# Kernel tuning notes

Hardware: AMD Instinct MI355X
Metric: run time of the kernel (lower is better)

Reference implementation:

```python
import jax, jax.numpy as jnp
import numpy as np

N = 500_000          # total nodes (25000 graphs x 20 joints)
E = 800_000          # total edges (25000 graphs x 32 edges)
NUM_EDGES = 32       # edges per graph (module init arg)
IN_C = 128
OUT_C = 256
LN_EPS = 1e-5


def setup_inputs() -> dict:
    key = jax.random.key(0)
    ks = jax.random.split(key, 8)
    x = jax.random.normal(ks[0], (N, IN_C), dtype=jnp.float32)
    edge_index = jax.random.randint(ks[1], (2, E), 0, N, dtype=jnp.int64)
    # learned per-graph edge weights (init ones in torch; randomized positive here)
    edge_weights = jax.random.uniform(ks[2], (NUM_EDGES,), jnp.float32, 0.5, 1.5)
    W_gcn = jax.random.normal(ks[3], (IN_C, OUT_C), jnp.float32) / np.float32(np.sqrt(IN_C))
    b_gcn = jnp.zeros((OUT_C,), jnp.float32)
    W_res = jax.random.normal(ks[4], (IN_C, OUT_C), jnp.float32) / np.float32(np.sqrt(IN_C))
    b_res = jnp.zeros((OUT_C,), jnp.float32)
    gamma = jnp.ones((OUT_C,), jnp.float32)
    beta = jnp.zeros((OUT_C,), jnp.float32)
    return dict(x=x, edge_weights=edge_weights, W_gcn=W_gcn, b_gcn=b_gcn,
                W_res=W_res, b_res=b_res, gamma=gamma, beta=beta,
                edge_index=edge_index)


def reference(x, edge_weights, W_gcn, b_gcn, W_res, b_res, gamma, beta, edge_index):
    n = x.shape[0]
    e_tot = edge_index.shape[1]
    batch_size = e_tot // NUM_EDGES
    ew = jnp.tile(edge_weights, batch_size)            # repeated per-batch weights [E]
    row, col = edge_index[0], edge_index[1]            # source -> target

    # GCN symmetric normalization with implicit self loops (weight 1)
    deg = jax.ops.segment_sum(ew, col, num_segments=n) + 1.0   # [N]
    dinv = jax.lax.rsqrt(deg)                                   # [N]
    norm = dinv[row] * ew * dinv[col]                           # [E]

    xw = x @ W_gcn                                              # [N, OUT_C]
    agg = jax.ops.segment_sum(norm[:, None] * xw[row], col, num_segments=n)
    # self-loop contribution: norm_ii = dinv_i * 1 * dinv_i = 1/deg_i
    gcn_out = agg + xw * (dinv * dinv)[:, None] + b_gcn         # [N, OUT_C]

    res = x @ W_res + b_res                                     # residual Linear
    h = gcn_out + res

    mu = jnp.mean(h, axis=-1, keepdims=True)
    var = jnp.mean((h - mu) ** 2, axis=-1, keepdims=True)
    hn = (h - mu) * jax.lax.rsqrt(var + LN_EPS)
    return jax.nn.relu(hn * gamma + beta)
```

## Files before the change

### kernel.cpp

```cpp
#include <hip/hip_runtime.h>
#include <hip/hip_bf16.h>

typedef __attribute__((ext_vector_type(8))) short short8;
typedef __attribute__((ext_vector_type(8))) unsigned short ushort8;
typedef __attribute__((ext_vector_type(4))) float f32x4;
typedef unsigned short u16;

#define IN_C 128
#define OUT_C 256
#define LN_EPS 1e-5f

__device__ __forceinline__ u16 f2bf(float f) {
    __hip_bfloat16 h = __float2bfloat16(f);
    return __builtin_bit_cast(u16, h);
}

__global__ void k_count(const int* __restrict__ ei, const float* __restrict__ ew,
                        float* __restrict__ deg, int* __restrict__ cnt, int E, int nbc,
                        const float* __restrict__ Wg, const float* __restrict__ Wr,
                        const float* __restrict__ bg, const float* __restrict__ br,
                        u16* __restrict__ wfrag, float* __restrict__ bc) {
    int b = blockIdx.x;
    if (b < nbc) {
        int e = b * 256 + threadIdx.x;
        if (e < E) {
            int c = ei[E + e];
            atomicAdd(&deg[c], ew[e & 31]);
            atomicAdd(&cnt[c], 1);
        }
        return;
    }
    int tid = (b - nbc) * 256 + threadIdx.x;
    if (tid < OUT_C) bc[tid] = bg[tid] + br[tid];
    if (tid >= 8192) return;
    int l = tid & 63;
    int t = (tid >> 6) & 15;
    int s = tid >> 10;
    int n = t * 16 + (l & 15);
    int k0 = s * 32 + (l >> 4) * 8;
    short8 pk;
#pragma unroll
    for (int j = 0; j < 8; ++j) {
        int k = k0 + j;
        float w = (k < IN_C) ? Wg[k * OUT_C + n] : Wr[(k - IN_C) * OUT_C + n];
        pk[j] = (short)f2bf(w);
    }
    reinterpret_cast<short8*>(wfrag)[tid] = pk;
}

__global__ void k_scan1(const int* __restrict__ cnt, int* __restrict__ partial,
                        float* __restrict__ deg, int n) {
    __shared__ int sm[256];
    int b = blockIdx.x, t = threadIdx.x;
    int base = b * 1024 + t * 4;
    int s = 0;
#pragma unroll
    for (int k = 0; k < 4; ++k) {
        int i = base + k;
        if (i < n) { s += cnt[i]; deg[i] = rsqrtf(1.0f + deg[i]); }
    }
    sm[t] = s; __syncthreads();
    for (int m = 128; m > 0; m >>= 1) { if (t < m) sm[t] += sm[t + m]; __syncthreads(); }
    if (t == 0) partial[b] = sm[0];
}

__global__ void k_scan2(int* __restrict__ partial, int nb) {
    __shared__ int sm[512];
    int t = threadIdx.x;
    sm[t] = (t < nb) ? partial[t] : 0;
    __syncthreads();
    for (int d = 1; d < 512; d <<= 1) {
        int v = (t >= d) ? sm[t - d] : 0;
        __syncthreads();
        sm[t] += v;
        __syncthreads();
    }
    if (t < nb) partial[t] = (t == 0) ? 0 : sm[t - 1];
}

__global__ void k_scan3(const int* __restrict__ cnt, const int* __restrict__ partial,
                        int* __restrict__ off, int* __restrict__ cur, int n, int E) {
    __shared__ int sm[256];
    int b = blockIdx.x, t = threadIdx.x;
    int base = b * 1024 + t * 4;
    int c[4]; int s = 0;
#pragma unroll
    for (int k = 0; k < 4; ++k) { int i = base + k; c[k] = (i < n) ? cnt[i] : 0; s += c[k]; }
    sm[t] = s; __syncthreads();
    for (int d = 1; d < 256; d <<= 1) {
        int v = (t >= d) ? sm[t - d] : 0;
        __syncthreads();
        sm[t] += v;
        __syncthreads();
    }
    int run = partial[b] + (sm[t] - s);
#pragma unroll
    for (int k = 0; k < 4; ++k) {
        int i = base + k;
        if (i < n) { off[i] = run; cur[i] = run; }
        run += c[k];
    }
    if (b == 0 && t == 0) off[n] = E;
}

__global__ void k_place(const int* __restrict__ ei, const float* __restrict__ ew,
                        const float* __restrict__ dinv, int* __restrict__ cur,
                        int2* __restrict__ rec2, int E) {
    int e = blockIdx.x * 256 + threadIdx.x;
    if (e >= E) return;
    int r = ei[e], c = ei[E + e];
    float nrm = dinv[r] * ew[e & 31] * dinv[c];
    int p = atomicAdd(&cur[c], 1);
    rec2[p] = make_int2(r, __float_as_int(nrm));
}

__global__ __launch_bounds__(512, 4) void k_gemm(
    const float4* __restrict__ x4, const float* __restrict__ dinv,
    const int* __restrict__ off, const int2* __restrict__ rec2g,
    const u16* __restrict__ wfrag, const float* __restrict__ bc,
    const float* __restrict__ gamma, const float* __restrict__ beta,
    float* __restrict__ out, int N) {

    __shared__ u16 A[32 * 264];
    __shared__ float red[8 * 32 * 2];
    __shared__ float fin[32 * 2];

    const int tid = threadIdx.x;
    const int lane = tid & 63;
    const int wv = tid >> 6;
    const long r0 = (long)blockIdx.x * 32;

    const int trow = tid >> 4;
    const int tq = tid & 15;
    const long gr = r0 + trow;

    float ua[8];
    int p0 = 0, p1 = 0;
    {
        u16* xp = &A[trow * 264 + 128 + tq * 8];
        if (gr < N) {
            float d = dinv[gr];
            float d2 = d * d;
            const float4* xs = x4 + gr * 32 + tq * 2;
            float4 v0 = xs[0], v1 = xs[1];
            ushort8 xx;
            xx[0] = f2bf(v0.x); xx[1] = f2bf(v0.y); xx[2] = f2bf(v0.z); xx[3] = f2bf(v0.w);
            xx[4] = f2bf(v1.x); xx[5] = f2bf(v1.y); xx[6] = f2bf(v1.z); xx[7] = f2bf(v1.w);
            *reinterpret_cast<ushort8*>(xp) = xx;
            ua[0] = v0.x * d2; ua[1] = v0.y * d2; ua[2] = v0.z * d2; ua[3] = v0.w * d2;
            ua[4] = v1.x * d2; ua[5] = v1.y * d2; ua[6] = v1.z * d2; ua[7] = v1.w * d2;
            p0 = off[gr]; p1 = off[gr + 1];
        } else {
#pragma unroll
            for (int k = 0; k < 8; ++k) ua[k] = 0.f;
            ushort8 zz = {0, 0, 0, 0, 0, 0, 0, 0};
            *reinterpret_cast<ushort8*>(xp) = zz;
        }
    }

    for (int p = p0; p < p1; p += 4) {
        const int nb = p1 - p;
        int sr[4]; float nr[4];
        float4 ga[4][2];
#pragma unroll
        for (int b = 0; b < 4; ++b) {
            if (b < nb) {
                int2 rc = rec2g[p + b];
                sr[b] = rc.x;
                nr[b] = __int_as_float(rc.y);
            }
        }
#pragma unroll
        for (int b = 0; b < 4; ++b) {
            if (b < nb) {
                const float4* xr = x4 + (long)sr[b] * 32 + tq * 2;
                ga[b][0] = xr[0];
                ga[b][1] = xr[1];
            }
        }
#pragma unroll
        for (int b = 0; b < 4; ++b) {
            if (b < nb) {
                ua[0] += nr[b] * ga[b][0].x; ua[1] += nr[b] * ga[b][0].y;
                ua[2] += nr[b] * ga[b][0].z; ua[3] += nr[b] * ga[b][0].w;
                ua[4] += nr[b] * ga[b][1].x; ua[5] += nr[b] * ga[b][1].y;
                ua[6] += nr[b] * ga[b][1].z; ua[7] += nr[b] * ga[b][1].w;
            }
        }
    }

    {
        ushort8 uu;
        uu[0] = f2bf(ua[0]); uu[1] = f2bf(ua[1]); uu[2] = f2bf(ua[2]); uu[3] = f2bf(ua[3]);
        uu[4] = f2bf(ua[4]); uu[5] = f2bf(ua[5]); uu[6] = f2bf(ua[6]); uu[7] = f2bf(ua[7]);
        u16* up = &A[trow * 264 + tq * 8];
        *reinterpret_cast<ushort8*>(up) = uu;
    }
    __syncthreads();

    const short8* wf = reinterpret_cast<const short8*>(wfrag);
    short8 bfr[8][2];
#pragma unroll
    for (int s = 0; s < 8; ++s) {
#pragma unroll
        for (int t = 0; t < 2; ++t)
            bfr[s][t] = wf[(s * 16 + (wv * 2 + t)) * 64 + lane];
    }

    f32x4 acc[2][2];
#pragma unroll
    for (int m = 0; m < 2; ++m)
#pragma unroll
        for (int t = 0; t < 2; ++t) acc[m][t] = (f32x4){0.f, 0.f, 0.f, 0.f};

    const int arowb = lane & 15;
    const int koff = (lane >> 4) * 8;
#pragma unroll
    for (int s = 0; s < 8; ++s) {
#pragma unroll
        for (int m = 0; m < 2; ++m) {
            short8 af = *reinterpret_cast<const short8*>(
                &A[(m * 16 + arowb) * 264 + s * 32 + koff]);
#pragma unroll
            for (int t = 0; t < 2; ++t)
                acc[m][t] = __builtin_amdgcn_mfma_f32_16x16x32_bf16(af, bfr[s][t], acc[m][t], 0, 0, 0);
        }
    }

    const int ncol = lane & 15;
    const int g = lane >> 4;
    const float bc0 = bc[wv * 32 + ncol];
    const float bc1 = bc[wv * 32 + 16 + ncol];
#pragma unroll
    for (int m = 0; m < 2; ++m) {
#pragma unroll
        for (int j = 0; j < 4; ++j) {
            float v0 = acc[m][0][j] + bc0;
            float v1 = acc[m][1][j] + bc1;
            acc[m][0][j] = v0;
            acc[m][1][j] = v1;
            float s = v0 + v1;
            float q = v0 * v0 + v1 * v1;
#pragma unroll
            for (int msk = 1; msk < 16; msk <<= 1) {
                s += __shfl_xor(s, msk);
                q += __shfl_xor(q, msk);
            }
            if (ncol == 0) {
                int row = m * 16 + g * 4 + j;
                red[(wv * 32 + row) * 2 + 0] = s;
                red[(wv * 32 + row) * 2 + 1] = q;
            }
        }
    }
    __syncthreads();
    if (tid < 64) {
        int row = tid >> 1, q = tid & 1;
        float t = 0.f;
#pragma unroll
        for (int w = 0; w < 8; ++w) t += red[(w * 32 + row) * 2 + q];
        fin[row * 2 + q] = t;
    }
    __syncthreads();

    const float gv0 = gamma[wv * 32 + ncol], bv0 = beta[wv * 32 + ncol];
    const float gv1 = gamma[wv * 32 + 16 + ncol], bv1 = beta[wv * 32 + 16 + ncol];
#pragma unroll
    for (int m = 0; m < 2; ++m) {
#pragma unroll
        for (int j = 0; j < 4; ++j) {
            int row = m * 16 + g * 4 + j;
            long rr = r0 + row;
            if (rr < N) {
                float mean = fin[row * 2] * (1.f / 256.f);
                float var = fin[row * 2 + 1] * (1.f / 256.f) - mean * mean;
                float rstd = rsqrtf(var + LN_EPS);
                float o0 = (acc[m][0][j] - mean) * rstd * gv0 + bv0;
                float o1 = (acc[m][1][j] - mean) * rstd * gv1 + bv1;
                float* op = out + rr * (long)OUT_C + wv * 32 + ncol;
                op[0]  = fmaxf(o0, 0.f);
                op[16] = fmaxf(o1, 0.f);
            }
        }
    }
}

extern "C" void kernel_launch(void* const* d_in, const int* in_sizes, int n_in,
                              void* d_out, int out_size, void* d_ws, size_t ws_size,
                              hipStream_t stream) {
    const float* x    = (const float*)d_in[0];
    const float* ew   = (const float*)d_in[1];
    const float* Wg   = (const float*)d_in[2];
    const float* bg   = (const float*)d_in[3];
    const float* Wr   = (const float*)d_in[4];
    const float* br   = (const float*)d_in[5];
    const float* gm   = (const float*)d_in[6];
    const float* bt   = (const float*)d_in[7];
    const int*   ei   = (const int*)d_in[8];

    const int N = in_sizes[0] / IN_C;
    const int E = in_sizes[8] / 2;
    const int NB1 = (N + 1023) / 1024;
    const int NBC = (E + 255) / 256;

    int2*  rec2 = (int2*)d_ws;
    float* deg  = (float*)(rec2 + E);
    int*   cnt  = (int*)(deg + N);
    int*   off  = cnt + N;
    int*   cur  = off + N + 1;
    int*   part = cur + N;
    u16*   wfrag = (u16*)(part + 512);
    float* bc   = (float*)(wfrag + 65536);

    hipMemsetAsync(deg, 0, (size_t)N * sizeof(float), stream);
    hipMemsetAsync(cnt, 0, (size_t)N * sizeof(int), stream);
    k_count<<<NBC + 32, 256, 0, stream>>>(ei, ew, deg, cnt, E, NBC,
                                          Wg, Wr, bg, br, wfrag, bc);
    k_scan1<<<NB1, 256, 0, stream>>>(cnt, part, deg, N);
    k_scan2<<<1, 512, 0, stream>>>(part, NB1);
    k_scan3<<<NB1, 256, 0, stream>>>(cnt, part, off, cur, N, E);
    k_place<<<(E + 255) / 256, 256, 0, stream>>>(ei, ew, deg, cur, rec2, E);
    k_gemm<<<(N + 31) / 32, 512, 0, stream>>>((const float4*)x, deg, off, rec2,
                                              wfrag, bc, gm, bt, (float*)d_out, N);
}
```

Baseline: 462.5 us.

## Pack degree and count into one 64-bit atomic and shrink GEMM tile to 16 rows

Degree counting now issues one 64-bit atomicAdd per edge, packing the count into the high word and the edge weight as fixed point (scaled by 2^20) into the low word. Two memsets become one zeroing kernel. The fused gather-GEMM kernel now uses 256-thread blocks of 16 rows. Each wave streams its B fragments from global memory per MFMA instead of holding them in registers, and each block stages its edge records through shared memory in 256-entry chunks. This trades half the atomics and lower register pressure for fixed-point rounding of the degree, extra barriers, and B fragments being reloaded for every block.

```diff
diff --git a/kernel.cpp b/kernel.cpp
--- a/kernel.cpp
+++ b/kernel.cpp
@@ -5,18 +5,26 @@
 typedef __attribute__((ext_vector_type(8))) unsigned short ushort8;
 typedef __attribute__((ext_vector_type(4))) float f32x4;
 typedef unsigned short u16;
+typedef unsigned long long u64;
 
 #define IN_C 128
 #define OUT_C 256
 #define LN_EPS 1e-5f
+#define CHUNK 256
+#define WSCALE 1048576.0f
 
 __device__ __forceinline__ u16 f2bf(float f) {
     __hip_bfloat16 h = __float2bfloat16(f);
     return __builtin_bit_cast(u16, h);
 }
 
+__global__ void k_zero(float4* __restrict__ p, int n4) {
+    int i = blockIdx.x * 256 + threadIdx.x;
+    if (i < n4) p[i] = make_float4(0.f, 0.f, 0.f, 0.f);
+}
+
 __global__ void k_count(const int* __restrict__ ei, const float* __restrict__ ew,
-                        float* __restrict__ deg, int* __restrict__ cnt, int E, int nbc,
+                        u64* __restrict__ pk, int E, int nbc,
                         const float* __restrict__ Wg, const float* __restrict__ Wr,
                         const float* __restrict__ bg, const float* __restrict__ br,
                         u16* __restrict__ wfrag, float* __restrict__ bc) {
@@ -25,8 +33,8 @@
         int e = b * 256 + threadIdx.x;
         if (e < E) {
             int c = ei[E + e];
-            atomicAdd(&deg[c], ew[e & 31]);
-            atomicAdd(&cnt[c], 1);
+            unsigned w = (unsigned)(ew[e & 31] * WSCALE + 0.5f);
+            atomicAdd(&pk[c], (1ULL << 32) | (u64)w);
         }
         return;
     }
@@ -38,18 +46,18 @@
     int s = tid >> 10;
     int n = t * 16 + (l & 15);
     int k0 = s * 32 + (l >> 4) * 8;
-    short8 pk;
+    short8 pkk;
 #pragma unroll
     for (int j = 0; j < 8; ++j) {
         int k = k0 + j;
         float w = (k < IN_C) ? Wg[k * OUT_C + n] : Wr[(k - IN_C) * OUT_C + n];
-        pk[j] = (short)f2bf(w);
-    }
-    reinterpret_cast<short8*>(wfrag)[tid] = pk;
-}
-
-__global__ void k_scan1(const int* __restrict__ cnt, int* __restrict__ partial,
-                        float* __restrict__ deg, int n) {
+        pkk[j] = (short)f2bf(w);
+    }
+    reinterpret_cast<short8*>(wfrag)[tid] = pkk;
+}
+
+__global__ void k_scan1(const u64* __restrict__ pk, int* __restrict__ partial,
+                        float* __restrict__ dinv, int n) {
     __shared__ int sm[256];
     int b = blockIdx.x, t = threadIdx.x;
     int base = b * 1024 + t * 4;
@@ -57,7 +65,11 @@
 #pragma unroll
     for (int k = 0; k < 4; ++k) {
         int i = base + k;
-        if (i < n) { s += cnt[i]; deg[i] = rsqrtf(1.0f + deg[i]); }
+        if (i < n) {
+            u64 v = pk[i];
+            s += (int)(v >> 32);
+            dinv[i] = rsqrtf(1.0f + (float)(unsigned)(v & 0xffffffffULL) * (1.0f / WSCALE));
+        }
     }
     sm[t] = s; __syncthreads();
     for (int m = 128; m > 0; m >>= 1) { if (t < m) sm[t] += sm[t + m]; __syncthreads(); }
@@ -78,14 +90,18 @@
     if (t < nb) partial[t] = (t == 0) ? 0 : sm[t - 1];
 }
 
-__global__ void k_scan3(const int* __restrict__ cnt, const int* __restrict__ partial,
+__global__ void k_scan3(const u64* __restrict__ pk, const int* __restrict__ partial,
                         int* __restrict__ off, int* __restrict__ cur, int n, int E) {
     __shared__ int sm[256];
     int b = blockIdx.x, t = threadIdx.x;
     int base = b * 1024 + t * 4;
     int c[4]; int s = 0;
 #pragma unroll
-    for (int k = 0; k < 4; ++k) { int i = base + k; c[k] = (i < n) ? cnt[i] : 0; s += c[k]; }
+    for (int k = 0; k < 4; ++k) {
+        int i = base + k;
+        c[k] = (i < n) ? (int)(pk[i] >> 32) : 0;
+        s += c[k];
+    }
     sm[t] = s; __syncthreads();
     for (int d = 1; d < 256; d <<= 1) {
         int v = (t >= d) ? sm[t - d] : 0;
@@ -114,21 +130,22 @@
     rec2[p] = make_int2(r, __float_as_int(nrm));
 }
 
-__global__ __launch_bounds__(512, 4) void k_gemm(
+__global__ __launch_bounds__(256, 8) void k_gemm(
     const float4* __restrict__ x4, const float* __restrict__ dinv,
     const int* __restrict__ off, const int2* __restrict__ rec2g,
     const u16* __restrict__ wfrag, const float* __restrict__ bc,
     const float* __restrict__ gamma, const float* __restrict__ beta,
     float* __restrict__ out, int N) {
 
-    __shared__ u16 A[32 * 264];
-    __shared__ float red[8 * 32 * 2];
-    __shared__ float fin[32 * 2];
+    __shared__ u16 A[16 * 264];
+    __shared__ float red[4 * 16 * 2];
+    __shared__ float fin[16 * 2];
+    __shared__ int2 recs[CHUNK];
 
     const int tid = threadIdx.x;
     const int lane = tid & 63;
     const int wv = tid >> 6;
-    const long r0 = (long)blockIdx.x * 32;
+    const long r0 = (long)blockIdx.x * 16;
 
     const int trow = tid >> 4;
     const int tq = tid & 15;
@@ -158,33 +175,44 @@
         }
     }
 
-    for (int p = p0; p < p1; p += 4) {
-        const int nb = p1 - p;
-        int sr[4]; float nr[4];
-        float4 ga[4][2];
-#pragma unroll
-        for (int b = 0; b < 4; ++b) {
-            if (b < nb) {
-                int2 rc = rec2g[p + b];
-                sr[b] = rc.x;
-                nr[b] = __int_as_float(rc.y);
+    const int rend = (int)((r0 + 16 < N) ? (r0 + 16) : N);
+    const int e0 = off[r0];
+    const int e1 = off[rend];
+    for (int cb = e0; cb < e1; cb += CHUNK) {
+        const int ce = (cb + CHUNK < e1) ? (cb + CHUNK) : e1;
+        __syncthreads();
+        for (int i = tid; i < ce - cb; i += 256) recs[i] = rec2g[cb + i];
+        __syncthreads();
+        const int q0 = (p0 > cb) ? p0 : cb;
+        const int q1 = (p1 < ce) ? p1 : ce;
+        for (int p = q0; p < q1; p += 4) {
+            const int nb = q1 - p;
+            int sr[4]; float nr[4];
+            float4 ga[4][2];
+#pragma unroll
+            for (int b = 0; b < 4; ++b) {
+                if (b < nb) {
+                    int2 rc = recs[p - cb + b];
+                    sr[b] = rc.x;
+                    nr[b] = __int_as_float(rc.y);
+                }
             }
-        }
-#pragma unroll
-        for (int b = 0; b < 4; ++b) {
-            if (b < nb) {
-                const float4* xr = x4 + (long)sr[b] * 32 + tq * 2;
-                ga[b][0] = xr[0];
-                ga[b][1] = xr[1];
+#pragma unroll
+            for (int b = 0; b < 4; ++b) {
+                if (b < nb) {
+                    const float4* xr = x4 + (long)sr[b] * 32 + tq * 2;
+                    ga[b][0] = xr[0];
+                    ga[b][1] = xr[1];
+                }
             }
-        }
-#pragma unroll
-        for (int b = 0; b < 4; ++b) {
-            if (b < nb) {
-                ua[0] += nr[b] * ga[b][0].x; ua[1] += nr[b] * ga[b][0].y;
-                ua[2] += nr[b] * ga[b][0].z; ua[3] += nr[b] * ga[b][0].w;
-                ua[4] += nr[b] * ga[b][1].x; ua[5] += nr[b] * ga[b][1].y;
-                ua[6] += nr[b] * ga[b][1].z; ua[7] += nr[b] * ga[b][1].w;
+#pragma unroll
+            for (int b = 0; b < 4; ++b) {
+                if (b < nb) {
+                    ua[0] += nr[b] * ga[b][0].x; ua[1] += nr[b] * ga[b][0].y;
+                    ua[2] += nr[b] * ga[b][0].z; ua[3] += nr[b] * ga[b][0].w;
+                    ua[4] += nr[b] * ga[b][1].x; ua[5] += nr[b] * ga[b][1].y;
+                    ua[6] += nr[b] * ga[b][1].z; ua[7] += nr[b] * ga[b][1].w;
+                }
             }
         }
     }
@@ -198,88 +226,78 @@
     }
     __syncthreads();
 
-    const short8* wf = reinterpret_cast<const short8*>(wfrag);
-    short8 bfr[8][2];
-#pragma unroll
-    for (int s = 0; s < 8; ++s) {
-#pragma unroll
-        for (int t = 0; t < 2; ++t)
-            bfr[s][t] = wf[(s * 16 + (wv * 2 + t)) * 64 + lane];
-    }
-
-    f32x4 acc[2][2];
-#pragma unroll
-    for (int m = 0; m < 2; ++m)
-#pragma unroll
-        for (int t = 0; t < 2; ++t) acc[m][t] = (f32x4){0.f, 0.f, 0.f, 0.f};
+    f32x4 acc[4];
+#pragma unroll
+    for (int t = 0; t < 4; ++t) acc[t] = (f32x4){0.f, 0.f, 0.f, 0.f};
 
     const int arowb = lane & 15;
     const int koff = (lane >> 4) * 8;
+    const short8* wf = reinterpret_cast<const short8*>(wfrag);
 #pragma unroll
     for (int s = 0; s < 8; ++s) {
-#pragma unroll
-        for (int m = 0; m < 2; ++m) {
-            short8 af = *reinterpret_cast<const short8*>(
-                &A[(m * 16 + arowb) * 264 + s * 32 + koff]);
-#pragma unroll
-            for (int t = 0; t < 2; ++t)
-                acc[m][t] = __builtin_amdgcn_mfma_f32_16x16x32_bf16(af, bfr[s][t], acc[m][t], 0, 0, 0);
+        short8 af = *reinterpret_cast<const short8*>(&A[arowb * 264 + s * 32 + koff]);
+#pragma unroll
+        for (int t = 0; t < 4; ++t) {
+            short8 bfr = wf[(s * 16 + (wv * 4 + t)) * 64 + lane];
+            acc[t] = __builtin_amdgcn_mfma_f32_16x16x32_bf16(af, bfr, acc[t], 0, 0, 0);
         }
     }
 
     const int ncol = lane & 15;
     const int g = lane >> 4;
-    const float bc0 = bc[wv * 32 + ncol];
-    const float bc1 = bc[wv * 32 + 16 + ncol];
-#pragma unroll
-    for (int m = 0; m < 2; ++m) {
-#pragma unroll
-        for (int j = 0; j < 4; ++j) {
-            float v0 = acc[m][0][j] + bc0;
-            float v1 = acc[m][1][j] + bc1;
-            acc[m][0][j] = v0;
-            acc[m][1][j] = v1;
-            float s = v0 + v1;
-            float q = v0 * v0 + v1 * v1;
-#pragma unroll
-            for (int msk = 1; msk < 16; msk <<= 1) {
-                s += __shfl_xor(s, msk);
-                q += __shfl_xor(q, msk);
-            }
-            if (ncol == 0) {
-                int row = m * 16 + g * 4 + j;
-                red[(wv * 32 + row) * 2 + 0] = s;
-                red[(wv * 32 + row) * 2 + 1] = q;
-            }
+    float bcv[4];
+#pragma unroll
+    for (int t = 0; t < 4; ++t) bcv[t] = bc[wv * 64 + t * 16 + ncol];
+#pragma unroll
+    for (int j = 0; j < 4; ++j) {
+        float s = 0.f, q = 0.f;
+#pragma unroll
+        for (int t = 0; t < 4; ++t) {
+            float v = acc[t][j] + bcv[t];
+            acc[t][j] = v;
+            s += v;
+            q += v * v;
+        }
+#pragma unroll
+        for (int msk = 1; msk < 16; msk <<= 1) {
+            s += __shfl_xor(s, msk);
+            q += __shfl_xor(q, msk);
+        }
+        if (ncol == 0) {
+            int row = g * 4 + j;
+            red[(wv * 16 + row) * 2 + 0] = s;
+            red[(wv * 16 + row) * 2 + 1] = q;
         }
     }
     __syncthreads();
-    if (tid < 64) {
+    if (tid < 32) {
         int row = tid >> 1, q = tid & 1;
         float t = 0.f;
 #pragma unroll
-        for (int w = 0; w < 8; ++w) t += red[(w * 32 + row) * 2 + q];
+        for (int w = 0; w < 4; ++w) t += red[(w * 16 + row) * 2 + q];
         fin[row * 2 + q] = t;
     }
     __syncthreads();
 
-    const float gv0 = gamma[wv * 32 + ncol], bv0 = beta[wv * 32 + ncol];
-    const float gv1 = gamma[wv * 32 + 16 + ncol], bv1 = beta[wv * 32 + 16 + ncol];
-#pragma unroll
-    for (int m = 0; m < 2; ++m) {
-#pragma unroll
-        for (int j = 0; j < 4; ++j) {
-            int row = m * 16 + g * 4 + j;
-            long rr = r0 + row;
-            if (rr < N) {
-                float mean = fin[row * 2] * (1.f / 256.f);
-                float var = fin[row * 2 + 1] * (1.f / 256.f) - mean * mean;
-                float rstd = rsqrtf(var + LN_EPS);
-                float o0 = (acc[m][0][j] - mean) * rstd * gv0 + bv0;
-                float o1 = (acc[m][1][j] - mean) * rstd * gv1 + bv1;
-                float* op = out + rr * (long)OUT_C + wv * 32 + ncol;
-                op[0]  = fmaxf(o0, 0.f);
-                op[16] = fmaxf(o1, 0.f);
+    float gv[4], bv[4];
+#pragma unroll
+    for (int t = 0; t < 4; ++t) {
+        gv[t] = gamma[wv * 64 + t * 16 + ncol];
+        bv[t] = beta[wv * 64 + t * 16 + ncol];
+    }
+#pragma unroll
+    for (int j = 0; j < 4; ++j) {
+        int row = g * 4 + j;
+        long rr = r0 + row;
+        if (rr < N) {
+            float mean = fin[row * 2] * (1.f / 256.f);
+            float var = fin[row * 2 + 1] * (1.f / 256.f) - mean * mean;
+            float rstd = rsqrtf(var + LN_EPS);
+            float* op = out + rr * (long)OUT_C + wv * 64 + ncol;
+#pragma unroll
+            for (int t = 0; t < 4; ++t) {
+                float o = (acc[t][j] - mean) * rstd * gv[t] + bv[t];
+                op[t * 16] = fmaxf(o, 0.f);
             }
         }
     }
@@ -304,22 +322,22 @@
     const int NBC = (E + 255) / 256;
 
     int2*  rec2 = (int2*)d_ws;
-    float* deg  = (float*)(rec2 + E);
-    int*   cnt  = (int*)(deg + N);
-    int*   off  = cnt + N;
+    u64*   pk   = (u64*)(rec2 + E);
+    float* dinv = (float*)(pk + N);
+    int*   off  = (int*)(dinv + N);
     int*   cur  = off + N + 1;
     int*   part = cur + N;
     u16*   wfrag = (u16*)(part + 512);
     float* bc   = (float*)(wfrag + 65536);
 
-    hipMemsetAsync(deg, 0, (size_t)N * sizeof(float), stream);
-    hipMemsetAsync(cnt, 0, (size_t)N * sizeof(int), stream);
-    k_count<<<NBC + 32, 256, 0, stream>>>(ei, ew, deg, cnt, E, NBC,
+    const int n4 = (2 * N + 3) / 4;
+    k_zero<<<(n4 + 255) / 256, 256, 0, stream>>>((float4*)pk, n4);
+    k_count<<<NBC + 32, 256, 0, stream>>>(ei, ew, pk, E, NBC,
                                           Wg, Wr, bg, br, wfrag, bc);
-    k_scan1<<<NB1, 256, 0, stream>>>(cnt, part, deg, N);
+    k_scan1<<<NB1, 256, 0, stream>>>(pk, part, dinv, N);
     k_scan2<<<1, 512, 0, stream>>>(part, NB1);
-    k_scan3<<<NB1, 256, 0, stream>>>(cnt, part, off, cur, N, E);
-    k_place<<<(E + 255) / 256, 256, 0, stream>>>(ei, ew, deg, cur, rec2, E);
-    k_gemm<<<(N + 31) / 32, 512, 0, stream>>>((const float4*)x, deg, off, rec2,
+    k_scan3<<<NB1, 256, 0, stream>>>(pk, part, off, cur, N, E);
+    k_place<<<(E + 255) / 256, 256, 0, stream>>>(ei, ew, dinv, cur, rec2, E);
+    k_gemm<<<(N + 15) / 16, 256, 0, stream>>>((const float4*)x, dinv, off, rec2,
                                               wfrag, bc, gm, bt, (float*)d_out, N);
 }
```

Result: slower. 500.5 us (+8.2%).
